# Optimization experiments

Measured on AMD Instinct MI355X. Metric: run time of the kernel, lower is better.

The kernel has to match this reference:

```python
import jax, jax.numpy as jnp
import numpy as np

N_HEADS = 16

def _apply_rope(x, cos, sin):
    # x: [B, S, H, D]; cos/sin: [S, D//2]
    B, S, H, D = x.shape
    half = D // 2
    x1, x2 = x[..., :half], x[..., half:]
    c = cos[:S, None, :]  # [S, 1, half] -> broadcast over heads
    s = sin[:S, None, :]
    o1 = x1 * c - x2 * s
    o2 = x1 * s + x2 * c
    return jnp.concatenate([o1, o2], axis=-1).astype(x.dtype)


def setup_inputs() -> dict:
    key = jax.random.key(0)
    ks = jax.random.split(key, 6)
    B, S, dim = 2, 2048, 2048
    head_dim = dim // N_HEADS
    half = head_dim // 2
    x = jax.random.normal(ks[0], (B, S, dim), dtype=jnp.float32)
    # real RoPE tables (theta=10000)
    inv_freq = 1.0 / (10000.0 ** (np.arange(0, half, dtype=np.float32) / half))
    t = np.arange(S, dtype=np.float32)
    freqs = np.outer(t, inv_freq)  # [S, half]
    cos = jnp.asarray(np.cos(freqs), dtype=jnp.float32)
    sin = jnp.asarray(np.sin(freqs), dtype=jnp.float32)
    scale = 0.02
    wq = jax.random.normal(ks[1], (dim, dim), dtype=jnp.float32) * scale
    wk = jax.random.normal(ks[2], (dim, dim), dtype=jnp.float32) * scale
    wv = jax.random.normal(ks[3], (dim, dim), dtype=jnp.float32) * scale
    wo = jax.random.normal(ks[4], (dim, dim), dtype=jnp.float32) * scale
    return {"x": x, "cos": cos, "sin": sin, "wq": wq, "wk": wk, "wv": wv, "wo": wo}


def reference(x, cos, sin, wq, wk, wv, wo):
    B, S, dim = x.shape
    H = N_HEADS
    Dh = dim // H
    # QKV projections (nn.Linear: x @ W.T)
    q = (x @ wq.T).reshape(B, S, H, Dh)
    k = (x @ wk.T).reshape(B, S, H, Dh)
    v = (x @ wv.T).reshape(B, S, H, Dh)
    q = _apply_rope(q, cos, sin)
    k = _apply_rope(k, cos, sin)
    # causal attention (flash_attn_func with causal=True, dropout 0 in eval)
    scores = jnp.einsum('bqhd,bkhd->bhqk', q, k) / jnp.sqrt(jnp.asarray(Dh, x.dtype))
    causal = jnp.tril(jnp.ones((S, S), dtype=bool))
    scores = jnp.where(causal, scores, jnp.asarray(-1e30, x.dtype))
    attn = jax.nn.softmax(scores, axis=-1)
    out = jnp.einsum('bhqk,bkhd->bqhd', attn, v).reshape(B, S, dim)
    return out @ wo.T
```

## Files before the change

kernel.cpp:

```cpp
#include <hip/hip_runtime.h>

typedef short short8 __attribute__((ext_vector_type(8)));
typedef float f32x4 __attribute__((ext_vector_type(4)));
typedef unsigned short ushort_t;

__device__ __forceinline__ unsigned short f2bf(float f){
  unsigned int u = __builtin_bit_cast(unsigned int, f);
  u += 0x7FFFu + ((u >> 16) & 1u);
  return (unsigned short)(u >> 16);
}
__device__ __forceinline__ float bf2f(unsigned short u){
  return __builtin_bit_cast(float, ((unsigned int)u) << 16);
}
__device__ __forceinline__ void gload_lds16(const void* g, void* l){
  __builtin_amdgcn_global_load_lds((const __attribute__((address_space(1))) unsigned int*)g,
                                   (__attribute__((address_space(3))) unsigned int*)l, 16, 0, 0);
}

__global__ __launch_bounds__(256) void cast_bf16_kernel(const float* __restrict__ in,
                                                        ushort_t* __restrict__ out, long n4){
  long i = (long)blockIdx.x*256 + threadIdx.x;
  if (i >= n4) return;
  const float4 v = reinterpret_cast<const float4*>(in)[i];
  ushort4 o; o.x=f2bf(v.x); o.y=f2bf(v.y); o.z=f2bf(v.z); o.w=f2bf(v.w);
  reinterpret_cast<ushort4*>(out)[i] = o;
}

__global__ __launch_bounds__(256) void cast4_bf16_kernel(const float* __restrict__ w0, const float* __restrict__ w1,
                                                         const float* __restrict__ w2, const float* __restrict__ w3,
                                                         ushort_t* __restrict__ o0, ushort_t* __restrict__ o1,
                                                         ushort_t* __restrict__ o2, ushort_t* __restrict__ o3,
                                                         long n4){
  long i = (long)blockIdx.x*256 + threadIdx.x;
  if (i >= n4) return;
  const float* in; ushort_t* out;
  switch (blockIdx.y){
    case 0: in = w0; out = o0; break;
    case 1: in = w1; out = o1; break;
    case 2: in = w2; out = o2; break;
    default: in = w3; out = o3; break;
  }
  const float4 v = reinterpret_cast<const float4*>(in)[i];
  ushort4 o; o.x=f2bf(v.x); o.y=f2bf(v.y); o.z=f2bf(v.z); o.w=f2bf(v.w);
  reinterpret_cast<ushort4*>(out)[i] = o;
}

__global__ __launch_bounds__(256) void rope2_kernel(ushort_t* __restrict__ Qs,
                                                    ushort_t* __restrict__ Ks,
                                                    const float* __restrict__ cosb,
                                                    const float* __restrict__ sinb){
  long idx = (long)blockIdx.x*256 + threadIdx.x;
  ushort_t* X = blockIdx.y ? Ks : Qs;
  const float scale = blockIdx.y ? 1.0f : 0.08838834764831845f;
  int dq = (int)(idx & 15);
  long rest = idx >> 4;
  int h = (int)(rest & 15); rest >>= 4;
  int s = (int)(rest & 2047);
  int b = (int)(rest >> 11);
  long base = ((long)(b*2048 + s))*2048 + h*128;
  int d0 = dq*4;
  ushort4 x1 = *(const ushort4*)&X[base + d0];
  ushort4 x2 = *(const ushort4*)&X[base + 64 + d0];
  float4 cc = *(const float4*)&cosb[s*64 + d0];
  float4 ss = *(const float4*)&sinb[s*64 + d0];
  ushort4 o1, o2;
  { float a=bf2f(x1.x), bb=bf2f(x2.x); o1.x=f2bf((a*cc.x-bb*ss.x)*scale); o2.x=f2bf((a*ss.x+bb*cc.x)*scale); }
  { float a=bf2f(x1.y), bb=bf2f(x2.y); o1.y=f2bf((a*cc.y-bb*ss.y)*scale); o2.y=f2bf((a*ss.y+bb*cc.y)*scale); }
  { float a=bf2f(x1.z), bb=bf2f(x2.z); o1.z=f2bf((a*cc.z-bb*ss.z)*scale); o2.z=f2bf((a*ss.z+bb*cc.z)*scale); }
  { float a=bf2f(x1.w), bb=bf2f(x2.w); o1.w=f2bf((a*cc.w-bb*ss.w)*scale); o2.w=f2bf((a*ss.w+bb*cc.w)*scale); }
  *(ushort4*)&X[base + d0] = o1;
  *(ushort4*)&X[base + 64 + d0] = o2;
}

#define LDA8(DST, P, QM) do{ \
  _Pragma("unroll") for (int i_ = 0; i_ < 4; ++i_){ \
    DST[i_][0] = *(const short8*)&lA[(P)*16384 + ((QM)*128 + aRowBase + i_*16)*64 + sw0]; \
    DST[i_][1] = *(const short8*)&lA[(P)*16384 + ((QM)*128 + aRowBase + i_*16)*64 + sw1]; } }while(0)

#define LDB4(DST, P, BH) do{ \
  _Pragma("unroll") for (int j_ = 0; j_ < 2; ++j_){ \
    DST[j_][0] = *(const short8*)&lB[(P)*16384 + ((BH)*128 + bRowBase + j_*16)*64 + sw0]; \
    DST[j_][1] = *(const short8*)&lB[(P)*16384 + ((BH)*128 + bRowBase + j_*16)*64 + sw1]; } }while(0)

#define STAGE_A(P, QM, T) do{ \
  gload_lds16(aS0 + (long)(QM)*64*K + (long)(T)*64, &lA[(P)*16384 + (QM)*8192 + tid*8]); \
  gload_lds16(aS1 + (long)(QM)*64*K + (long)(T)*64, &lA[(P)*16384 + (QM)*8192 + 4096 + tid*8]); }while(0)

#define STAGE_B(P, QN, T) do{ \
  gload_lds16(bS0 + (long)(QN)*32*K + (long)(T)*64, &lB[(P)*16384 + (QN)*8192 + tid*8]); \
  gload_lds16(bS1 + (long)(QN)*32*K + (long)(T)*64, &lB[(P)*16384 + (QN)*8192 + 4096 + tid*8]); }while(0)

#define MFK(QM, BH, AR, BR) do{ \
  __builtin_amdgcn_s_setprio(1); \
  _Pragma("unroll") for (int k_ = 0; k_ < 2; ++k_) \
    _Pragma("unroll") for (int i_ = 0; i_ < 4; ++i_) \
      _Pragma("unroll") for (int j_ = 0; j_ < 2; ++j_) \
        acc[(QM)*4+i_][(BH)*2+j_] = __builtin_amdgcn_mfma_f32_16x16x32_bf16(AR[i_][k_], BR[j_][k_], acc[(QM)*4+i_][(BH)*2+j_], 0, 0, 0); \
  __builtin_amdgcn_s_setprio(0); }while(0)

#define BAR() do{ __builtin_amdgcn_s_barrier(); asm volatile("" ::: "memory"); }while(0)
#define VM(N) asm volatile("s_waitcnt vmcnt(" #N ")" ::: "memory")

__global__ __launch_bounds__(512, 2) void gemm_qkv_8ph(const ushort_t* __restrict__ A,
                                                       const ushort_t* __restrict__ Bw,
                                                       ushort_t* __restrict__ Cq,
                                                       ushort_t* __restrict__ Ck,
                                                       ushort_t* __restrict__ Vt,
                                                       int MT, int K){
  __shared__ ushort_t lA[32768];
  __shared__ ushort_t lB[32768];
  const int tid = threadIdx.x;
  const int lane = tid & 63, wid = tid >> 6;
  const int g = lane >> 4, c = lane & 15;
  const int wm = wid >> 2, wn = wid & 3;

  const int nwg = (int)gridDim.x, cpx = nwg >> 3;
  int sw = (blockIdx.x & 7)*cpx + (blockIdx.x >> 3);
  const long m0 = (long)(sw % MT)*256;
  const long n0 = (long)(sw / MT)*256;

  const int prl0 = tid >> 3, q1 = 512 + tid, prl1 = q1 >> 3;
  const int sl0 = ((tid & 7) ^ (prl0 & 7)) * 8;
  const int sl1 = ((q1 & 7) ^ (prl1 & 7)) * 8;
  const int rowA0 = ((prl0 >> 6)*128) + (prl0 & 63);
  const int rowA1 = ((prl1 >> 6)*128) + (prl1 & 63);
  const int rowB0 = ((prl0 >> 5)*64) + (prl0 & 31);
  const int rowB1 = ((prl1 >> 5)*64) + (prl1 & 31);
  const ushort_t* aS0 = A + (m0 + rowA0)*K + sl0;
  const ushort_t* aS1 = A + (m0 + rowA1)*K + sl1;
  const ushort_t* bS0 = Bw + (n0 + rowB0)*K + sl0;
  const ushort_t* bS1 = Bw + (n0 + rowB1)*K + sl1;

  const int sw0 = (g ^ (c & 7)) * 8;
  const int sw1 = ((4 + g) ^ (c & 7)) * 8;
  const int aRowBase = wm*64 + c;
  const int bRowBase = wn*32 + c;

  f32x4 acc[8][4] = {};
  short8 aR[4][2], aR2[4][2], b0[2][2], b1[2][2];
  const int NI = K >> 7;

  STAGE_A(0, 0, 0); STAGE_B(0, 0, 0);
  STAGE_B(0, 1, 0); STAGE_A(0, 1, 0);
  STAGE_A(1, 0, 1); STAGE_B(1, 0, 1); STAGE_B(1, 1, 1);
  VM(6);
  BAR();

  for (int j = 0; j < NI-1; ++j){
    const int t = 2*j;
     LDA8(aR, 0, 0); LDB4(b0, 0, 0); STAGE_A(1, 1, t+1); BAR(); MFK(0, 0, aR, b0); BAR();
     LDB4(b1, 0, 1);                 STAGE_A(0, 0, t+2); BAR(); MFK(0, 1, aR, b1); BAR();
     LDA8(aR2, 0, 1);                STAGE_B(0, 0, t+2); BAR(); MFK(1, 0, aR2, b0); BAR();
     VM(4);                          STAGE_B(0, 1, t+2); BAR(); MFK(1, 1, aR2, b1); BAR();
     LDA8(aR, 1, 0); LDB4(b0, 1, 0); STAGE_A(0, 1, t+2); BAR(); MFK(0, 0, aR, b0); BAR();
     LDB4(b1, 1, 1);                 STAGE_A(1, 0, t+3); BAR(); MFK(0, 1, aR, b1); BAR();
     LDA8(aR2, 1, 1);                STAGE_B(1, 0, t+3); BAR(); MFK(1, 0, aR2, b0); BAR();
     VM(4);                          STAGE_B(1, 1, t+3); BAR(); MFK(1, 1, aR2, b1); BAR();
  }
  {
    const int t = 2*(NI-1);
     LDA8(aR, 0, 0); LDB4(b0, 0, 0); STAGE_A(1, 1, t+1); BAR(); MFK(0, 0, aR, b0); BAR();
     LDB4(b1, 0, 1);                                     BAR(); MFK(0, 1, aR, b1); BAR();
     LDA8(aR2, 0, 1);                                    BAR(); MFK(1, 0, aR2, b0); BAR();
     VM(0);                                              BAR(); MFK(1, 1, aR2, b1); BAR();
     LDA8(aR, 1, 0); LDB4(b0, 1, 0);                     BAR(); MFK(0, 0, aR, b0); BAR();
     LDB4(b1, 1, 1);                                     BAR(); MFK(0, 1, aR, b1); BAR();
     LDA8(aR2, 1, 1);                                    BAR(); MFK(1, 0, aR2, b0); BAR();
                                                         BAR(); MFK(1, 1, aR2, b1); BAR();
  }

  const long rbase = m0 + wm*128 + g*4;
  const long cbase = n0 + wn*64 + c;
  const int third = (int)(n0 >> 11);
  if (third < 2){
    ushort_t* dst = (third == 0) ? Cq : Ck;
    const long csub = cbase - (long)third*2048;
#pragma unroll
    for (int mi = 0; mi < 8; ++mi)
#pragma unroll
      for (int ni = 0; ni < 4; ++ni){
        long off = (rbase + mi*16)*2048 + csub + ni*16;
#pragma unroll
        for (int r = 0; r < 4; ++r)
          dst[off + (long)r*2048] = f2bf(acc[mi][ni][r]);
      }
  } else {
#pragma unroll
    for (int mi = 0; mi < 8; ++mi){
      const long row = rbase + mi*16;
      const long s = row & 2047, bb = row >> 11;
#pragma unroll
      for (int ni = 0; ni < 4; ++ni){
        long hd = cbase + ni*16 - 4096;
        long vaddr = ((bb*16 + (hd >> 7))*128 + (hd & 127))*2048 + s;
        ushort4 o4;
        o4.x = f2bf(acc[mi][ni][0]); o4.y = f2bf(acc[mi][ni][1]);
        o4.z = f2bf(acc[mi][ni][2]); o4.w = f2bf(acc[mi][ni][3]);
        *(ushort4*)&Vt[vaddr] = o4;
      }
    }
  }
}


#define WLDA8(P) do{ \
  _Pragma("unroll") for (int i_ = 0; i_ < 4; ++i_){ \
    aF[i_][0] = *(const short8*)&lA[(P)*8192 + (wm*64 + i_*16 + c)*64 + sw0]; \
    aF[i_][1] = *(const short8*)&lA[(P)*8192 + (wm*64 + i_*16 + c)*64 + sw1]; } }while(0)

#define WLDB4(P, NH) do{ \
  _Pragma("unroll") for (int j_ = 0; j_ < 2; ++j_){ \
    bF[j_][0] = *(const short8*)&lB[(P)*16384 + (wn*64 + ((NH)*2+j_)*16 + c)*64 + sw0]; \
    bF[j_][1] = *(const short8*)&lB[(P)*16384 + (wn*64 + ((NH)*2+j_)*16 + c)*64 + sw1]; } }while(0)

#define WSTAGE_A(P, T) do{ \
  gload_lds16(aW + (long)(T)*64,          &lA[(P)*8192 + tid*8]); \
  gload_lds16(aW + 64l*K + (long)(T)*64,  &lA[(P)*8192 + 4096 + tid*8]); }while(0)

#define WSTAGE_B0(P, T) do{ \
  gload_lds16(bW + (long)(T)*64,          &lB[(P)*16384 + tid*8]); \
  gload_lds16(bW + 64l*K + (long)(T)*64,  &lB[(P)*16384 + 4096 + tid*8]); }while(0)

#define WSTAGE_B1(P, T) do{ \
  gload_lds16(bW + 128l*K + (long)(T)*64, &lB[(P)*16384 + 8192 + tid*8]); \
  gload_lds16(bW + 192l*K + (long)(T)*64, &lB[(P)*16384 + 12288 + tid*8]); }while(0)

#define WMF16(NH) do{ \
  __builtin_amdgcn_s_setprio(1); \
  _Pragma("unroll") for (int k_ = 0; k_ < 2; ++k_) \
    _Pragma("unroll") for (int i_ = 0; i_ < 4; ++i_) \
      _Pragma("unroll") for (int j_ = 0; j_ < 2; ++j_) \
        acc[i_][(NH)*2+j_] = __builtin_amdgcn_mfma_f32_16x16x32_bf16(aF[i_][k_], bF[j_][k_], acc[i_][(NH)*2+j_], 0, 0, 0); \
  __builtin_amdgcn_s_setprio(0); }while(0)

__global__ __launch_bounds__(512, 2) void gemm_wo_8ph(const ushort_t* __restrict__ A,
                                                      const ushort_t* __restrict__ Bw,
                                                      float* __restrict__ C,
                                                      int MT, int N, int K){
  __shared__ ushort_t lA[16384];
  __shared__ ushort_t lB[32768];
  const int tid = threadIdx.x;
  const int lane = tid & 63, wid = tid >> 6;
  const int g = lane >> 4, c = lane & 15;
  const int wm = wid >> 2, wn = wid & 3;

  const int nwg = (int)gridDim.x, cpx = nwg >> 3;
  int sw = (blockIdx.x & 7)*cpx + (blockIdx.x >> 3);
  const long m0 = (long)(sw % MT)*128;
  const long n0 = (long)(sw / MT)*256;

  const int rr = tid >> 3;
  const int ss = ((tid & 7) ^ (rr & 7)) * 8;
  const ushort_t* aW = A + (m0 + rr)*K + ss;
  const ushort_t* bW = Bw + (n0 + rr)*K + ss;

  const int sw0 = (g ^ (c & 7)) * 8;
  const int sw1 = ((4 + g) ^ (c & 7)) * 8;

  f32x4 acc[4][4] = {};
  short8 aF[4][2], bF[2][2];
  const int NI = K >> 7;

  WSTAGE_A(0, 0); WSTAGE_B0(0, 0); WSTAGE_B1(0, 0);
  WSTAGE_A(1, 1);
  VM(2);
  BAR();

  for (int j = 0; j < NI-1; ++j){
    const int t = 2*j;
     WLDA8(0); WLDB4(0, 0); WSTAGE_B0(1, t+1); WSTAGE_B1(1, t+1); BAR(); WMF16(0); BAR();
     WLDB4(0, 1); VM(0); WSTAGE_A(0, t+2);                        BAR(); WMF16(1); BAR();
     WLDA8(1); WLDB4(1, 0); WSTAGE_B0(0, t+2); WSTAGE_B1(0, t+2); BAR(); WMF16(0); BAR();
     WLDB4(1, 1); VM(0); WSTAGE_A(1, t+3);                        BAR(); WMF16(1); BAR();
  }
  {
    const int t = 2*(NI-1);
     WLDA8(0); WLDB4(0, 0); WSTAGE_B0(1, t+1); WSTAGE_B1(1, t+1); BAR(); WMF16(0); BAR();
     WLDB4(0, 1); VM(0);                                          BAR(); WMF16(1); BAR();
     WLDA8(1); WLDB4(1, 0);                                       BAR(); WMF16(0); BAR();
     WLDB4(1, 1);                                                 BAR(); WMF16(1); BAR();
  }

#pragma unroll
  for (int i = 0; i < 4; ++i)
#pragma unroll
    for (int jn = 0; jn < 4; ++jn){
      long off = (m0 + wm*64 + i*16 + g*4)*(long)N + n0 + wn*64 + jn*16 + c;
#pragma unroll
      for (int r = 0; r < 4; ++r)
        C[off + (long)r*N] = acc[i][jn][r];
    }
}

__global__ __launch_bounds__(256) void attn_kernel(const ushort_t* __restrict__ Q,
                                                   const ushort_t* __restrict__ Kr,
                                                   const ushort_t* __restrict__ Vt,
                                                   ushort_t* __restrict__ O){
  const int tid = threadIdx.x;
  const int l = tid & 63, w = tid >> 6;
  const int g = l >> 4, c = l & 15;
  const int bh = blockIdx.x;
  const int qt = (int)gridDim.y - 1 - (int)blockIdx.y;
  const int b = bh >> 4, h = bh & 15;
  const int q0 = qt * 64;
  const int qw0 = q0 + w * 16;
  const int nt = qt + 1;

  __shared__ ushort_t k_lds[2][64*128];
  __shared__ ushort_t v_lds[2][128*64];
  __shared__ ushort_t p_lds[4][16*72];

  short8 qf[4];
  const long qbase = ((long)(b*2048 + qw0 + c))*2048 + h*128 + g*8;
#pragma unroll
  for (int ds = 0; ds < 4; ++ds) qf[ds] = *(const short8*)(Q + qbase + ds*32);

  const ushort_t* ksrc[4]; const ushort_t* vsrc[4];
  int kof[4], vof[4];
#pragma unroll
  for (int i = 0; i < 4; ++i){
    int q = i*256 + tid;
    int r = q >> 4, j = q & 15;
    ksrc[i] = Kr + ((long)(b*2048 + r))*2048 + h*128 + (j ^ (r & 7))*8;
    kof[i] = q*8;
    int d = q >> 3, jj = q & 7;
    vsrc[i] = Vt + ((long)(bh*128 + d))*2048 + (jj ^ (d & 7))*8;
    vof[i] = q*8;
  }

  f32x4 o[8] = {};
  float m = -1e30f, lsum = 0.f;
  const int sw = (c & 7) << 3;

#pragma unroll
  for (int i = 0; i < 4; ++i) gload_lds16(ksrc[i], &k_lds[0][kof[i]]);
#pragma unroll
  for (int i = 0; i < 4; ++i) gload_lds16(vsrc[i], &v_lds[0][vof[i]]);
  __syncthreads();

  for (int t = 0; t < nt; ++t){
    const int p = t & 1;
    if (t + 1 < nt){
#pragma unroll
      for (int i = 0; i < 4; ++i)
        gload_lds16(ksrc[i] + (long)(t+1)*64*2048, &k_lds[p^1][kof[i]]);
#pragma unroll
      for (int i = 0; i < 4; ++i)
        gload_lds16(vsrc[i] + (t+1)*64, &v_lds[p^1][vof[i]]);
    }
    const int kv0 = t*64;

    f32x4 s[4] = {};
    __builtin_amdgcn_s_setprio(1);
#pragma unroll
    for (int t4 = 0; t4 < 4; ++t4){
      const int row = 16*t4 + c;
#pragma unroll
      for (int ds = 0; ds < 4; ++ds){
        short8 kf = *(const short8*)&k_lds[p][(row*128 + ds*32 + g*8) ^ sw];
        s[t4] = __builtin_amdgcn_mfma_f32_16x16x32_bf16(kf, qf[ds], s[t4], 0, 0, 0);
      }
    }
    __builtin_amdgcn_s_setprio(0);
    if (kv0 + 63 > qw0){
      const int qg = qw0 + c;
#pragma unroll
      for (int t4 = 0; t4 < 4; ++t4)
#pragma unroll
        for (int r = 0; r < 4; ++r)
          if (kv0 + 16*t4 + 4*g + r > qg) s[t4][r] = -1e30f;
    }
    float tm = -1e30f;
#pragma unroll
    for (int t4 = 0; t4 < 4; ++t4)
      tm = fmaxf(tm, fmaxf(fmaxf(s[t4][0], s[t4][1]), fmaxf(s[t4][2], s[t4][3])));
    tm = fmaxf(tm, __shfl_xor(tm, 16, 64));
    tm = fmaxf(tm, __shfl_xor(tm, 32, 64));
    if (!__all(tm <= m + 8.f)){
      float mn = fmaxf(m, tm);
      float al = __expf(m - mn);
      m = mn;
      lsum *= al;
      float alr[4];
#pragma unroll
      for (int r = 0; r < 4; ++r) alr[r] = __shfl(al, 4*g + r, 64);
#pragma unroll
      for (int dt = 0; dt < 8; ++dt)
#pragma unroll
        for (int r = 0; r < 4; ++r) o[dt][r] *= alr[r];
    }
    float ps = 0.f;
#pragma unroll
    for (int t4 = 0; t4 < 4; ++t4)
#pragma unroll
      for (int r = 0; r < 4; ++r){ float pex = __expf(s[t4][r] - m); s[t4][r] = pex; ps += pex; }
    ps += __shfl_xor(ps, 16, 64);
    ps += __shfl_xor(ps, 32, 64);
    lsum += ps;
#pragma unroll
    for (int t4 = 0; t4 < 4; ++t4){
      uint2 pw;
      pw.x = (unsigned)f2bf(s[t4][0]) | ((unsigned)f2bf(s[t4][1]) << 16);
      pw.y = (unsigned)f2bf(s[t4][2]) | ((unsigned)f2bf(s[t4][3]) << 16);
      *reinterpret_cast<uint2*>(&p_lds[w][c*72 + 16*t4 + 4*g]) = pw;
    }
    __builtin_amdgcn_s_setprio(1);
#pragma unroll
    for (int kc = 0; kc < 2; ++kc){
      short8 pf = *(const short8*)&p_lds[w][c*72 + 32*kc + 8*g];
#pragma unroll
      for (int dt = 0; dt < 8; ++dt){
        short8 vf = *(const short8*)&v_lds[p][(((16*dt + c)*64) + kc*32 + g*8) ^ sw];
        o[dt] = __builtin_amdgcn_mfma_f32_16x16x32_bf16(pf, vf, o[dt], 0, 0, 0);
      }
    }
    __builtin_amdgcn_s_setprio(0);
    __syncthreads();
  }

  float inv = 1.f / lsum;
  float invr[4];
#pragma unroll
  for (int r = 0; r < 4; ++r) invr[r] = __shfl(inv, 4*g + r, 64);
  const long obase = ((long)(b*2048 + qw0 + g*4))*2048 + h*128 + c;
#pragma unroll
  for (int dt = 0; dt < 8; ++dt)
#pragma unroll
    for (int r = 0; r < 4; ++r)
      O[obase + (long)r*2048 + dt*16] = f2bf(o[dt][r] * invr[r]);
}

extern "C" void kernel_launch(void* const* d_in, const int* in_sizes, int n_in,
                              void* d_out, int out_size, void* d_ws, size_t ws_size,
                              hipStream_t stream){
  const float* x    = (const float*)d_in[0];
  const float* cosb = (const float*)d_in[1];
  const float* sinb = (const float*)d_in[2];
  const float* wq   = (const float*)d_in[3];
  const float* wk   = (const float*)d_in[4];
  const float* wv   = (const float*)d_in[5];
  const float* wo   = (const float*)d_in[6];
  float* out = (float*)d_out;

  const int S = 2048, DIM = 2048;
  const long MN = 4096;

  char* ws = (char*)d_ws;
  ushort_t* xb     = (ushort_t*)(ws);
  ushort_t* wqkvb  = (ushort_t*)(ws + (16l<<20));
  ushort_t* wob    = (ushort_t*)(ws + (40l<<20));
  ushort_t* qstage = (ushort_t*)(ws + (48l<<20));
  ushort_t* kstage = (ushort_t*)(ws + (64l<<20));
  ushort_t* attnb  = (ushort_t*)(ws + (80l<<20));
  ushort_t* vt     = (ushort_t*)(ws + (96l<<20));

  const long xn4 = MN*DIM/4, wn4 = (long)DIM*DIM/4;
  cast_bf16_kernel<<<(int)((xn4+255)/256), 256, 0, stream>>>(x, xb, xn4);
  cast4_bf16_kernel<<<dim3((int)((wn4+255)/256), 4), 256, 0, stream>>>(
      wq, wk, wv, wo,
      wqkvb, wqkvb + 4194304, wqkvb + 8388608, wob, wn4);

  gemm_qkv_8ph<<<(MN/256)*(6144/256), 512, 0, stream>>>(
      xb, wqkvb, qstage, kstage, vt, (int)(MN/256), DIM);

  const int ropeBlocks = (2*2048*16*16)/256;
  rope2_kernel<<<dim3(ropeBlocks, 2), 256, 0, stream>>>(qstage, kstage, cosb, sinb);
  attn_kernel<<<dim3(32, S/64), 256, 0, stream>>>(qstage, kstage, vt, attnb);
  gemm_wo_8ph<<<(MN/128)*(DIM/256), 512, 0, stream>>>(attnb, wob, out, (int)(MN/128), DIM, DIM);
}
```

Measured before the change: 275.2 us.

## Replace 256x256 QKV GEMM with 128x256 tile using shared W-core pipeline

The QKV projection GEMM moves from a 256x256 tile with an 8-phase schedule to the 128x256 tile and 4-phase pipeline already used by the output projection. The shared main loop becomes a macro so both GEMMs use it. The grid doubles to 768 workgroups, which should fill the CUs more evenly and reduce LDS use per block. In exchange, each tile has lower arithmetic intensity, so the A/B operands are reloaded more often.

```diff
diff --git a/kernel.cpp b/kernel.cpp
--- a/kernel.cpp
+++ b/kernel.cpp
@@ -72,136 +72,9 @@
   *(ushort4*)&X[base + 64 + d0] = o2;
 }
 
-#define LDA8(DST, P, QM) do{ \
-  _Pragma("unroll") for (int i_ = 0; i_ < 4; ++i_){ \
-    DST[i_][0] = *(const short8*)&lA[(P)*16384 + ((QM)*128 + aRowBase + i_*16)*64 + sw0]; \
-    DST[i_][1] = *(const short8*)&lA[(P)*16384 + ((QM)*128 + aRowBase + i_*16)*64 + sw1]; } }while(0)
-
-#define LDB4(DST, P, BH) do{ \
-  _Pragma("unroll") for (int j_ = 0; j_ < 2; ++j_){ \
-    DST[j_][0] = *(const short8*)&lB[(P)*16384 + ((BH)*128 + bRowBase + j_*16)*64 + sw0]; \
-    DST[j_][1] = *(const short8*)&lB[(P)*16384 + ((BH)*128 + bRowBase + j_*16)*64 + sw1]; } }while(0)
-
-#define STAGE_A(P, QM, T) do{ \
-  gload_lds16(aS0 + (long)(QM)*64*K + (long)(T)*64, &lA[(P)*16384 + (QM)*8192 + tid*8]); \
-  gload_lds16(aS1 + (long)(QM)*64*K + (long)(T)*64, &lA[(P)*16384 + (QM)*8192 + 4096 + tid*8]); }while(0)
-
-#define STAGE_B(P, QN, T) do{ \
-  gload_lds16(bS0 + (long)(QN)*32*K + (long)(T)*64, &lB[(P)*16384 + (QN)*8192 + tid*8]); \
-  gload_lds16(bS1 + (long)(QN)*32*K + (long)(T)*64, &lB[(P)*16384 + (QN)*8192 + 4096 + tid*8]); }while(0)
-
-#define MFK(QM, BH, AR, BR) do{ \
-  __builtin_amdgcn_s_setprio(1); \
-  _Pragma("unroll") for (int k_ = 0; k_ < 2; ++k_) \
-    _Pragma("unroll") for (int i_ = 0; i_ < 4; ++i_) \
-      _Pragma("unroll") for (int j_ = 0; j_ < 2; ++j_) \
-        acc[(QM)*4+i_][(BH)*2+j_] = __builtin_amdgcn_mfma_f32_16x16x32_bf16(AR[i_][k_], BR[j_][k_], acc[(QM)*4+i_][(BH)*2+j_], 0, 0, 0); \
-  __builtin_amdgcn_s_setprio(0); }while(0)
 
 #define BAR() do{ __builtin_amdgcn_s_barrier(); asm volatile("" ::: "memory"); }while(0)
 #define VM(N) asm volatile("s_waitcnt vmcnt(" #N ")" ::: "memory")
-
-__global__ __launch_bounds__(512, 2) void gemm_qkv_8ph(const ushort_t* __restrict__ A,
-                                                       const ushort_t* __restrict__ Bw,
-                                                       ushort_t* __restrict__ Cq,
-                                                       ushort_t* __restrict__ Ck,
-                                                       ushort_t* __restrict__ Vt,
-                                                       int MT, int K){
-  __shared__ ushort_t lA[32768];
-  __shared__ ushort_t lB[32768];
-  const int tid = threadIdx.x;
-  const int lane = tid & 63, wid = tid >> 6;
-  const int g = lane >> 4, c = lane & 15;
-  const int wm = wid >> 2, wn = wid & 3;
-
-  const int nwg = (int)gridDim.x, cpx = nwg >> 3;
-  int sw = (blockIdx.x & 7)*cpx + (blockIdx.x >> 3);
-  const long m0 = (long)(sw % MT)*256;
-  const long n0 = (long)(sw / MT)*256;
-
-  const int prl0 = tid >> 3, q1 = 512 + tid, prl1 = q1 >> 3;
-  const int sl0 = ((tid & 7) ^ (prl0 & 7)) * 8;
-  const int sl1 = ((q1 & 7) ^ (prl1 & 7)) * 8;
-  const int rowA0 = ((prl0 >> 6)*128) + (prl0 & 63);
-  const int rowA1 = ((prl1 >> 6)*128) + (prl1 & 63);
-  const int rowB0 = ((prl0 >> 5)*64) + (prl0 & 31);
-  const int rowB1 = ((prl1 >> 5)*64) + (prl1 & 31);
-  const ushort_t* aS0 = A + (m0 + rowA0)*K + sl0;
-  const ushort_t* aS1 = A + (m0 + rowA1)*K + sl1;
-  const ushort_t* bS0 = Bw + (n0 + rowB0)*K + sl0;
-  const ushort_t* bS1 = Bw + (n0 + rowB1)*K + sl1;
-
-  const int sw0 = (g ^ (c & 7)) * 8;
-  const int sw1 = ((4 + g) ^ (c & 7)) * 8;
-  const int aRowBase = wm*64 + c;
-  const int bRowBase = wn*32 + c;
-
-  f32x4 acc[8][4] = {};
-  short8 aR[4][2], aR2[4][2], b0[2][2], b1[2][2];
-  const int NI = K >> 7;
-
-  STAGE_A(0, 0, 0); STAGE_B(0, 0, 0);
-  STAGE_B(0, 1, 0); STAGE_A(0, 1, 0);
-  STAGE_A(1, 0, 1); STAGE_B(1, 0, 1); STAGE_B(1, 1, 1);
-  VM(6);
-  BAR();
-
-  for (int j = 0; j < NI-1; ++j){
-    const int t = 2*j;
-     LDA8(aR, 0, 0); LDB4(b0, 0, 0); STAGE_A(1, 1, t+1); BAR(); MFK(0, 0, aR, b0); BAR();
-     LDB4(b1, 0, 1);                 STAGE_A(0, 0, t+2); BAR(); MFK(0, 1, aR, b1); BAR();
-     LDA8(aR2, 0, 1);                STAGE_B(0, 0, t+2); BAR(); MFK(1, 0, aR2, b0); BAR();
-     VM(4);                          STAGE_B(0, 1, t+2); BAR(); MFK(1, 1, aR2, b1); BAR();
-     LDA8(aR, 1, 0); LDB4(b0, 1, 0); STAGE_A(0, 1, t+2); BAR(); MFK(0, 0, aR, b0); BAR();
-     LDB4(b1, 1, 1);                 STAGE_A(1, 0, t+3); BAR(); MFK(0, 1, aR, b1); BAR();
-     LDA8(aR2, 1, 1);                STAGE_B(1, 0, t+3); BAR(); MFK(1, 0, aR2, b0); BAR();
-     VM(4);                          STAGE_B(1, 1, t+3); BAR(); MFK(1, 1, aR2, b1); BAR();
-  }
-  {
-    const int t = 2*(NI-1);
-     LDA8(aR, 0, 0); LDB4(b0, 0, 0); STAGE_A(1, 1, t+1); BAR(); MFK(0, 0, aR, b0); BAR();
-     LDB4(b1, 0, 1);                                     BAR(); MFK(0, 1, aR, b1); BAR();
-     LDA8(aR2, 0, 1);                                    BAR(); MFK(1, 0, aR2, b0); BAR();
-     VM(0);                                              BAR(); MFK(1, 1, aR2, b1); BAR();
-     LDA8(aR, 1, 0); LDB4(b0, 1, 0);                     BAR(); MFK(0, 0, aR, b0); BAR();
-     LDB4(b1, 1, 1);                                     BAR(); MFK(0, 1, aR, b1); BAR();
-     LDA8(aR2, 1, 1);                                    BAR(); MFK(1, 0, aR2, b0); BAR();
-                                                         BAR(); MFK(1, 1, aR2, b1); BAR();
-  }
-
-  const long rbase = m0 + wm*128 + g*4;
-  const long cbase = n0 + wn*64 + c;
-  const int third = (int)(n0 >> 11);
-  if (third < 2){
-    ushort_t* dst = (third == 0) ? Cq : Ck;
-    const long csub = cbase - (long)third*2048;
-#pragma unroll
-    for (int mi = 0; mi < 8; ++mi)
-#pragma unroll
-      for (int ni = 0; ni < 4; ++ni){
-        long off = (rbase + mi*16)*2048 + csub + ni*16;
-#pragma unroll
-        for (int r = 0; r < 4; ++r)
-          dst[off + (long)r*2048] = f2bf(acc[mi][ni][r]);
-      }
-  } else {
-#pragma unroll
-    for (int mi = 0; mi < 8; ++mi){
-      const long row = rbase + mi*16;
-      const long s = row & 2047, bb = row >> 11;
-#pragma unroll
-      for (int ni = 0; ni < 4; ++ni){
-        long hd = cbase + ni*16 - 4096;
-        long vaddr = ((bb*16 + (hd >> 7))*128 + (hd & 127))*2048 + s;
-        ushort4 o4;
-        o4.x = f2bf(acc[mi][ni][0]); o4.y = f2bf(acc[mi][ni][1]);
-        o4.z = f2bf(acc[mi][ni][2]); o4.w = f2bf(acc[mi][ni][3]);
-        *(ushort4*)&Vt[vaddr] = o4;
-      }
-    }
-  }
-}
-
 
 #define WLDA8(P) do{ \
   _Pragma("unroll") for (int i_ = 0; i_ < 4; ++i_){ \
@@ -232,6 +105,89 @@
       _Pragma("unroll") for (int j_ = 0; j_ < 2; ++j_) \
         acc[i_][(NH)*2+j_] = __builtin_amdgcn_mfma_f32_16x16x32_bf16(aF[i_][k_], bF[j_][k_], acc[i_][(NH)*2+j_], 0, 0, 0); \
   __builtin_amdgcn_s_setprio(0); }while(0)
+
+#define W_CORE_BODY() \
+  WSTAGE_A(0, 0); WSTAGE_B0(0, 0); WSTAGE_B1(0, 0); \
+  WSTAGE_A(1, 1); \
+  VM(2); \
+  BAR(); \
+  for (int j = 0; j < NI-1; ++j){ \
+    const int t = 2*j; \
+     WLDA8(0); WLDB4(0, 0); WSTAGE_B0(1, t+1); WSTAGE_B1(1, t+1); BAR(); WMF16(0); BAR(); \
+     WLDB4(0, 1); VM(0); WSTAGE_A(0, t+2);                        BAR(); WMF16(1); BAR(); \
+     WLDA8(1); WLDB4(1, 0); WSTAGE_B0(0, t+2); WSTAGE_B1(0, t+2); BAR(); WMF16(0); BAR(); \
+     WLDB4(1, 1); VM(0); WSTAGE_A(1, t+3);                        BAR(); WMF16(1); BAR(); \
+  } \
+  { \
+    const int t = 2*(NI-1); \
+     WLDA8(0); WLDB4(0, 0); WSTAGE_B0(1, t+1); WSTAGE_B1(1, t+1); BAR(); WMF16(0); BAR(); \
+     WLDB4(0, 1); VM(0);                                          BAR(); WMF16(1); BAR(); \
+     WLDA8(1); WLDB4(1, 0);                                       BAR(); WMF16(0); BAR(); \
+     WLDB4(1, 1);                                                 BAR(); WMF16(1); BAR(); \
+  }
+
+__global__ __launch_bounds__(512, 2) void gemm_qkv_4ph(const ushort_t* __restrict__ A,
+                                                       const ushort_t* __restrict__ Bw,
+                                                       ushort_t* __restrict__ Cq,
+                                                       ushort_t* __restrict__ Ck,
+                                                       ushort_t* __restrict__ Vt,
+                                                       int MT, int K){
+  __shared__ ushort_t lA[16384];
+  __shared__ ushort_t lB[32768];
+  const int tid = threadIdx.x;
+  const int lane = tid & 63, wid = tid >> 6;
+  const int g = lane >> 4, c = lane & 15;
+  const int wm = wid >> 2, wn = wid & 3;
+
+  const int nwg = (int)gridDim.x, cpx = nwg >> 3;
+  int sw = (blockIdx.x & 7)*cpx + (blockIdx.x >> 3);
+  const long m0 = (long)(sw % MT)*128;
+  const long n0 = (long)(sw / MT)*256;
+
+  const int rr = tid >> 3;
+  const int ss = ((tid & 7) ^ (rr & 7)) * 8;
+  const ushort_t* aW = A + (m0 + rr)*K + ss;
+  const ushort_t* bW = Bw + (n0 + rr)*K + ss;
+
+  const int sw0 = (g ^ (c & 7)) * 8;
+  const int sw1 = ((4 + g) ^ (c & 7)) * 8;
+
+  f32x4 acc[4][4] = {};
+  short8 aF[4][2], bF[2][2];
+  const int NI = K >> 7;
+
+  W_CORE_BODY();
+
+  const int third = (int)(n0 >> 11);
+  if (third < 2){
+    ushort_t* dst = (third == 0) ? Cq : Ck;
+#pragma unroll
+    for (int i = 0; i < 4; ++i)
+#pragma unroll
+      for (int jn = 0; jn < 4; ++jn){
+        long col = n0 - (long)third*2048 + wn*64 + jn*16 + c;
+        long off = (m0 + wm*64 + i*16 + g*4)*2048 + col;
+#pragma unroll
+        for (int r = 0; r < 4; ++r)
+          dst[off + (long)r*2048] = f2bf(acc[i][jn][r]);
+      }
+  } else {
+#pragma unroll
+    for (int i = 0; i < 4; ++i){
+      const long row0 = m0 + wm*64 + i*16 + g*4;
+      const long s = row0 & 2047, bb = row0 >> 11;
+#pragma unroll
+      for (int jn = 0; jn < 4; ++jn){
+        long hd = n0 - 4096 + wn*64 + jn*16 + c;
+        long vaddr = ((bb*16 + (hd >> 7))*128 + (hd & 127))*2048 + s;
+        ushort4 o4;
+        o4.x = f2bf(acc[i][jn][0]); o4.y = f2bf(acc[i][jn][1]);
+        o4.z = f2bf(acc[i][jn][2]); o4.w = f2bf(acc[i][jn][3]);
+        *(ushort4*)&Vt[vaddr] = o4;
+      }
+    }
+  }
+}
 
 __global__ __launch_bounds__(512, 2) void gemm_wo_8ph(const ushort_t* __restrict__ A,
                                                       const ushort_t* __restrict__ Bw,
@@ -261,25 +217,7 @@
   short8 aF[4][2], bF[2][2];
   const int NI = K >> 7;
 
-  WSTAGE_A(0, 0); WSTAGE_B0(0, 0); WSTAGE_B1(0, 0);
-  WSTAGE_A(1, 1);
-  VM(2);
-  BAR();
-
-  for (int j = 0; j < NI-1; ++j){
-    const int t = 2*j;
-     WLDA8(0); WLDB4(0, 0); WSTAGE_B0(1, t+1); WSTAGE_B1(1, t+1); BAR(); WMF16(0); BAR();
-     WLDB4(0, 1); VM(0); WSTAGE_A(0, t+2);                        BAR(); WMF16(1); BAR();
-     WLDA8(1); WLDB4(1, 0); WSTAGE_B0(0, t+2); WSTAGE_B1(0, t+2); BAR(); WMF16(0); BAR();
-     WLDB4(1, 1); VM(0); WSTAGE_A(1, t+3);                        BAR(); WMF16(1); BAR();
-  }
-  {
-    const int t = 2*(NI-1);
-     WLDA8(0); WLDB4(0, 0); WSTAGE_B0(1, t+1); WSTAGE_B1(1, t+1); BAR(); WMF16(0); BAR();
-     WLDB4(0, 1); VM(0);                                          BAR(); WMF16(1); BAR();
-     WLDA8(1); WLDB4(1, 0);                                       BAR(); WMF16(0); BAR();
-     WLDB4(1, 1);                                                 BAR(); WMF16(1); BAR();
-  }
+  W_CORE_BODY();
 
 #pragma unroll
   for (int i = 0; i < 4; ++i)
@@ -460,8 +398,8 @@
       wq, wk, wv, wo,
       wqkvb, wqkvb + 4194304, wqkvb + 8388608, wob, wn4);
 
-  gemm_qkv_8ph<<<(MN/256)*(6144/256), 512, 0, stream>>>(
-      xb, wqkvb, qstage, kstage, vt, (int)(MN/256), DIM);
+  gemm_qkv_4ph<<<(MN/128)*(6144/256), 512, 0, stream>>>(
+      xb, wqkvb, qstage, kstage, vt, (int)(MN/128), DIM);
 
   const int ropeBlocks = (2*2048*16*16)/256;
   rope2_kernel<<<dim3(ropeBlocks, 2), 256, 0, stream>>>(qstage, kstage, cosb, sinb);
```

Result: no change. 280.3 us (+1.9%).
